# Optimization experiments

Hardware: AMD Instinct MI355X
Metric: run time of the kernel (lower is better)

## Reference

```python
import math
import jax, jax.numpy as jnp
import numpy as np

N_HEAD = 16
ROPE_BASE = 10000.0


def _qk_norm(x, scale):
    # RMSNorm over head_dim, eps added inside sqrt as in the torch code
    norm = jnp.sqrt(jnp.mean(x.astype(jnp.float32) ** 2, axis=-1, keepdims=True) + 1e-6)
    return (x.astype(jnp.float32) / norm * scale).astype(x.dtype)


def _rope3d(q, k, coords, token_type):
    # q,k: [B,H,T,D]; coords: [B,T,3]; token_type: [B,T]
    # head_dim is split into 3 equal chunks, chunk i rotated by coords[...,i].
    # Tokens with token_type == 0 (e.g. text tokens) are left unrotated.
    B, H, T, D = q.shape
    d3 = D // 3
    half = d3 // 2
    inv_freq = ROPE_BASE ** (-jnp.arange(half, dtype=jnp.float32) / half)  # [half]

    def rotate(x):
        # x: [B,H,T,D] -> rotate each of the 3 axis-chunks
        chunks = []
        for a in range(3):
            xa = x[..., a * d3:(a + 1) * d3]                       # [B,H,T,d3]
            ang = coords[:, None, :, a, None] * inv_freq            # [B,1,T,half]
            cos, sin = jnp.cos(ang), jnp.sin(ang)
            x1, x2 = xa[..., :half], xa[..., half:]
            chunks.append(jnp.concatenate([x1 * cos - x2 * sin,
                                           x1 * sin + x2 * cos], axis=-1))
        rot = jnp.concatenate(chunks, axis=-1)
        apply = (token_type > 0)[:, None, :, None]                  # [B,1,T,1]
        return jnp.where(apply, rot, x)

    return rotate(q), rotate(k)


def setup_inputs() -> dict:
    key = jax.random.key(0)
    ks = jax.random.split(key, 5)
    B, T, C = 2, 2048, 1536
    D = C // N_HEAD
    return {
        "x": jax.random.normal(ks[0], (B, T, C), jnp.float32),
        "coords": jax.random.uniform(ks[1], (B, T, 3), jnp.float32) * 32.0,
        "token_type": jax.random.randint(ks[2], (B, T), 0, 2),
        "W_qkv": jax.random.normal(ks[3], (3 * C, C), jnp.float32) * (1.0 / math.sqrt(C)),
        "W_out": jax.random.normal(ks[4], (C, C), jnp.float32) * (1.0 / math.sqrt(C)),
        "q_scale": jnp.ones((D,), jnp.float32),
        "k_scale": jnp.ones((D,), jnp.float32),
    }


def reference(x, coords, token_type, W_qkv, W_out, q_scale, k_scale):
    B, T, C = x.shape
    H = N_HEAD
    D = C // H
    qkv = x @ W_qkv.T                                   # [B,T,3C]
    q, k, v = jnp.split(qkv, 3, axis=-1)
    q = q.reshape(B, T, H, D).transpose(0, 2, 1, 3)     # [B,H,T,D]
    k = k.reshape(B, T, H, D).transpose(0, 2, 1, 3)
    v = v.reshape(B, T, H, D).transpose(0, 2, 1, 3)
    q = _qk_norm(q, q_scale)
    k = _qk_norm(k, k_scale)
    q, k = _rope3d(q, k, coords, token_type)
    scale = 1.0 / math.sqrt(D)
    attn = jnp.einsum('bhqd,bhkd->bhqk', q, k) * scale  # [B,H,T,T]
    causal = jnp.tril(jnp.ones((T, T), bool))
    attn = jnp.where(causal, attn, -jnp.inf)
    attn = jax.nn.softmax(attn, axis=-1)
    out = jnp.einsum('bhqk,bhkd->bhqd', attn, v)        # [B,H,T,D]
    out = out.transpose(0, 2, 1, 3).reshape(B, T, C)
    return out @ W_out.T
```

## Files before the change

### kernel.cpp

```cpp
#include <hip/hip_runtime.h>
#include <stdint.h>
#include <stddef.h>


typedef __attribute__((ext_vector_type(8))) __bf16 bf16x8;
typedef __attribute__((ext_vector_type(4))) __bf16 bf16x4;
typedef __attribute__((ext_vector_type(4))) float  f32x4;

#define NB 2
#define NT 2048
#define NC 1536
#define NH 16
#define ND 96
#define NQKV 4608
#define NM 4096
#define NR_BLOCKS 16384

static __device__ __forceinline__ float fexp2(float x) {
#if __has_builtin(__builtin_amdgcn_exp2f)
  return __builtin_amdgcn_exp2f(x);
#else
  return exp2f(x);
#endif
}

static __device__ __forceinline__ void g2lds16(const void* g, void* l) {
  __builtin_amdgcn_global_load_lds(
      (const __attribute__((address_space(1))) void*)g,
      (__attribute__((address_space(3))) void*)l, 16, 0, 0);
}

__global__ __launch_bounds__(256) void cvt3_f32_bf16(
    const float4* __restrict__ sx, bf16x4* __restrict__ dx, int n4x,
    const float4* __restrict__ sw, bf16x4* __restrict__ dw, int n4w,
    const float4* __restrict__ so, bf16x4* __restrict__ do_) {
  int i = blockIdx.x * 256 + threadIdx.x;
  const float4* s;
  bf16x4* d;
  if (i < n4x)            { s = sx + i;               d = dx + i; }
  else if (i < n4x + n4w) { s = sw + (i - n4x);       d = dw + (i - n4x); }
  else                    { s = so + (i - n4x - n4w); d = do_ + (i - n4x - n4w); }
  float4 v = *s;
  bf16x4 o;
  o[0] = (__bf16)v.x; o[1] = (__bf16)v.y;
  o[2] = (__bf16)v.z; o[3] = (__bf16)v.w;
  *d = o;
}

#define BAR1() do { __builtin_amdgcn_s_barrier(); \
                    asm volatile("" ::: "memory"); } while (0)
#define BAR2() do { asm volatile("" ::: "memory"); \
                    __builtin_amdgcn_s_barrier(); } while (0)
#define WAITLGKM() do { asm volatile("s_waitcnt lgkmcnt(0)" ::: "memory"); \
                        __builtin_amdgcn_sched_barrier(0); } while (0)
#define WAITVM6() asm volatile("s_waitcnt vmcnt(6)" ::: "memory")
#define WAITVM5() asm volatile("s_waitcnt vmcnt(5)" ::: "memory")

template <int MH>
static __device__ __forceinline__ void readA2(
    bf16x8 (&aR)[2][2], const char* buf, int aro, int sk0, int sk1) {
#pragma unroll
  for (int i = 0; i < 2; ++i) {
    const char* p = buf + aro + (MH * 2 + i) * 2048;
    aR[i][0] = *(const bf16x8*)(p + sk0);
    aR[i][1] = *(const bf16x8*)(p + sk1);
  }
}
template <int NF0, int NN>
static __device__ __forceinline__ void readBN(
    bf16x8 (&bb)[NN][2], const char* buf, int bro, int sk0, int sk1) {
#pragma unroll
  for (int j = 0; j < NN; ++j) {
    const char* p = buf + bro + (NF0 + j) * 2048;
    bb[j][0] = *(const bf16x8*)(p + sk0);
    bb[j][1] = *(const bf16x8*)(p + sk1);
  }
}
template <int MH, int NF0, int NN>
static __device__ __forceinline__ void quadN(
    f32x4 (&acc)[4][9], const bf16x8 (&aR)[2][2], const bf16x8 (&bb)[NN][2]) {
  __builtin_amdgcn_s_setprio(1);
#pragma unroll
  for (int i = 0; i < 2; ++i)
#pragma unroll
    for (int j = 0; j < NN; ++j)
#pragma unroll
      for (int ks = 0; ks < 2; ++ks)
        acc[MH * 2 + i][NF0 + j] = __builtin_amdgcn_mfma_f32_16x16x32_bf16(
            aR[i][ks], bb[j][ks], acc[MH * 2 + i][NF0 + j], 0, 0, 0);
  __builtin_amdgcn_s_setprio(0);
}

__global__ __launch_bounds__(512, 2) void gemm1_8ph(
    const __bf16* __restrict__ A, const __bf16* __restrict__ Bw,
    __bf16* __restrict__ C, int M, int N, int K) {
  __shared__ __align__(16) char lds[139264];
  char* const A0 = lds;
  char* const A1 = lds + 32768;
  char* const B0 = lds + 65536;
  char* const B1 = lds + 102400;

  const int tid = threadIdx.x;
  const int l   = tid & 63;
  const int w   = tid >> 6;
  const int wm  = w >> 1;
  const int wn  = w & 1;
  const int lm  = l & 15;
  const int lq  = l >> 4;

  const int nnt = 16;
  const int nwg = gridDim.x * gridDim.y;
  const int lid = blockIdx.y * gridDim.x + blockIdx.x;
  const int swz = (lid & 7) * (nwg >> 3) + (lid >> 3);
  const int m0  = (swz / nnt) * 256;
  const int n0  = (swz % nnt) * 288;

  const int aro = (wm * 64 + lm) * 128;
  const int bro = (wn * 144 + lm) * 128;
  const int sk0 = ((lq) ^ (lm & 7)) * 16;
  const int sk1 = ((4 + lq) ^ (lm & 7)) * 16;

  const int ssl = ((l & 7) ^ ((l >> 3) & 7)) * 8;
  auto stageA = [&](int grow0, int k0, char* dst) {
#pragma unroll
    for (int q2 = 0; q2 < 2; ++q2) {
      const int c   = w * 2 + q2;
      const int row = c * 8 + (l >> 3);
      g2lds16(A + (size_t)(grow0 + row) * K + k0 + ssl, dst + c * 1024);
    }
  };
  auto stageB = [&](int grow0, int k0, char* dst) {
#pragma unroll
    for (int q2 = 0; q2 < 2; ++q2) {
      const int c   = w * 2 + q2;
      const int row = c * 8 + (l >> 3);
      g2lds16(Bw + (size_t)(grow0 + row) * K + k0 + ssl, dst + c * 1024);
    }
    if (w < 2) {
      const int c   = 16 + w;
      const int row = c * 8 + (l >> 3);
      g2lds16(Bw + (size_t)(grow0 + row) * K + k0 + ssl, dst + c * 1024);
    }
  };

  f32x4 acc[4][9] = {};
  bf16x8 aL[2][2], aH[2][2], b5[5][2], b4[4][2];

  stageA(m0,       0,  A0);
  stageA(m0 + 128, 0,  A0 + 16384);
  stageB(n0,       0,  B0);
  stageB(n0 + 144, 0,  B0 + 18432);
  stageA(m0,       64, A1);
  stageA(m0 + 128, 64, A1 + 16384);

  const int NIT = K >> 7;
  for (int it = 0; it < NIT; ++it) {
    const int kh  = it * 128 + 64;
    const int knl = it * 128 + 128;
    const int knh = it * 128 + 192;
    stageB(n0, kh, B1);
    WAITVM6();
    BAR1();
    readA2<0>(aL, A0, aro, sk0, sk1);
    readBN<0, 5>(b5, B0, bro, sk0, sk1);
    WAITLGKM();
    quadN<0, 0, 5>(acc, aL, b5);
    BAR2();
    stageB(n0 + 144, kh, B1 + 18432);
    BAR1();
    readA2<1>(aH, A0, aro, sk0, sk1);
    WAITLGKM();
    quadN<1, 0, 5>(acc, aH, b5);
    BAR2();
    stageA(m0, knl, A0);
    BAR1();
    readBN<5, 4>(b4, B0, bro, sk0, sk1);
    WAITLGKM();
    quadN<1, 5, 4>(acc, aH, b4);
    BAR2();
    stageA(m0 + 128, knl, A0 + 16384);
    BAR1();
    quadN<0, 5, 4>(acc, aL, b4);
    BAR2();
    stageB(n0, knl, B0);
    WAITVM6();
    BAR1();
    readA2<0>(aL, A1, aro, sk0, sk1);
    readBN<0, 5>(b5, B1, bro, sk0, sk1);
    WAITLGKM();
    quadN<0, 0, 5>(acc, aL, b5);
    BAR2();
    stageB(n0 + 144, knl, B0 + 18432);
    BAR1();
    readA2<1>(aH, A1, aro, sk0, sk1);
    WAITLGKM();
    quadN<1, 0, 5>(acc, aH, b5);
    BAR2();
    stageA(m0, knh, A1);
    BAR1();
    readBN<5, 4>(b4, B1, bro, sk0, sk1);
    WAITLGKM();
    quadN<1, 5, 4>(acc, aH, b4);
    BAR2();
    stageA(m0 + 128, knh, A1 + 16384);
    BAR1();
    quadN<0, 5, 4>(acc, aL, b4);
    BAR2();
  }

  const int r0 = lq * 4;
#pragma unroll
  for (int mf = 0; mf < 4; ++mf)
#pragma unroll
    for (int nf = 0; nf < 9; ++nf)
#pragma unroll
      for (int r = 0; r < 4; ++r) {
        const size_t row = (size_t)(m0 + wm * 64 + mf * 16 + r0 + r);
        const size_t col = (size_t)(n0 + wn * 144 + nf * 16 + lm);
        C[row * N + col] = (__bf16)acc[mf][nf][r];
      }
}

template <int MH, int NF0, int NN>
static __device__ __forceinline__ void g2quad(
    f32x4 (&acc)[4][3], const bf16x8 (&aR)[2][2], const bf16x8 (&bb)[NN][2]) {
  __builtin_amdgcn_s_setprio(1);
#pragma unroll
  for (int i = 0; i < 2; ++i)
#pragma unroll
    for (int j = 0; j < NN; ++j)
#pragma unroll
      for (int ks = 0; ks < 2; ++ks)
        acc[MH * 2 + i][NF0 + j] = __builtin_amdgcn_mfma_f32_16x16x32_bf16(
            aR[i][ks], bb[j][ks], acc[MH * 2 + i][NF0 + j], 0, 0, 0);
  __builtin_amdgcn_s_setprio(0);
}

__global__ __launch_bounds__(512, 2) void gemm2_8ph(
    const __bf16* __restrict__ A, const __bf16* __restrict__ Bw,
    float* __restrict__ C, int M, int N, int K) {
  __shared__ __align__(16) char lds[81920];
  char* const A0 = lds;
  char* const A1 = lds + 16384;
  char* const B0 = lds + 32768;
  char* const B1 = lds + 57344;

  const int tid = threadIdx.x;
  const int l   = tid & 63;
  const int w   = tid >> 6;
  const int wm  = w >> 2;
  const int wn  = w & 3;
  const int lm  = l & 15;
  const int lq  = l >> 4;

  const int nwg = gridDim.x * gridDim.y;
  const int lid = blockIdx.y * gridDim.x + blockIdx.x;
  const int swz = (lid & 7) * (nwg >> 3) + (lid >> 3);
  const int m0  = (swz / 8) * 128;
  const int n0  = (swz % 8) * 192;

  const int aro = (wm * 64 + lm) * 128;
  const int bro = (wn * 48 + lm) * 128;
  const int sk0 = ((lq) ^ (lm & 7)) * 16;
  const int sk1 = ((4 + lq) ^ (lm & 7)) * 16;

  const int ssl = ((l & 7) ^ ((l >> 3) & 7)) * 8;
  auto stageA = [&](int k0, char* dst) {
#pragma unroll
    for (int q2 = 0; q2 < 2; ++q2) {
      const int c   = w * 2 + q2;
      const int row = c * 8 + (l >> 3);
      g2lds16(A + (size_t)(m0 + row) * K + k0 + ssl, dst + c * 1024);
    }
  };
  auto stageB = [&](int k0, char* dst) {
#pragma unroll
    for (int q2 = 0; q2 < 3; ++q2) {
      const int c   = w * 3 + q2;
      const int row = c * 8 + (l >> 3);
      g2lds16(Bw + (size_t)(n0 + row) * K + k0 + ssl, dst + c * 1024);
    }
  };

  f32x4 acc[4][3] = {};
  bf16x8 aL[2][2], aH[2][2], bL[2][2], bH[1][2];

  stageA(0,  A0);
  stageB(0,  B0);
  stageA(64, A1);

  const int NIT = K >> 7;
  for (int it = 0; it < NIT; ++it) {
    const int kh  = it * 128 + 64;
    const int knl = it * 128 + 128;
    const int knh = it * 128 + 192;
    stageB(kh, B1);
    WAITVM5();
    BAR1();
    readA2<0>(aL, A0, aro, sk0, sk1);
    readBN<0, 2>(bL, B0, bro, sk0, sk1);
    WAITLGKM();
    g2quad<0, 0, 2>(acc, aL, bL);
    BAR2();
    BAR1();
    readA2<1>(aH, A0, aro, sk0, sk1);
    WAITLGKM();
    g2quad<1, 0, 2>(acc, aH, bL);
    BAR2();
    stageA(knl, A0);
    BAR1();
    readBN<2, 1>(bH, B0, bro, sk0, sk1);
    WAITLGKM();
    g2quad<1, 2, 1>(acc, aH, bH);
    BAR2();
    BAR1();
    g2quad<0, 2, 1>(acc, aL, bH);
    BAR2();
    stageB(knl, B0);
    WAITVM5();
    BAR1();
    readA2<0>(aL, A1, aro, sk0, sk1);
    readBN<0, 2>(bL, B1, bro, sk0, sk1);
    WAITLGKM();
    g2quad<0, 0, 2>(acc, aL, bL);
    BAR2();
    BAR1();
    readA2<1>(aH, A1, aro, sk0, sk1);
    WAITLGKM();
    g2quad<1, 0, 2>(acc, aH, bL);
    BAR2();
    stageA(knh, A1);
    BAR1();
    readBN<2, 1>(bH, B1, bro, sk0, sk1);
    WAITLGKM();
    g2quad<1, 2, 1>(acc, aH, bH);
    BAR2();
    BAR1();
    g2quad<0, 2, 1>(acc, aL, bH);
    BAR2();
  }

  const int r0 = lq * 4;
#pragma unroll
  for (int mf = 0; mf < 4; ++mf)
#pragma unroll
    for (int nf = 0; nf < 3; ++nf)
#pragma unroll
      for (int r = 0; r < 4; ++r) {
        const size_t row = (size_t)(m0 + wm * 64 + mf * 16 + r0 + r);
        const size_t col = (size_t)(n0 + wn * 48 + nf * 16 + lm);
        C[row * N + col] = acc[mf][nf][r];
      }
}

static __device__ __forceinline__ float rope_one(float v, float p, int d,
                                                 const float* c3) {
  const int a  = d >> 5;
  const int j  = d & 31;
  const int jj = j & 15;
  const float invf = fexp2((float)jj * -0.8304820237218406f);
  const float ang  = c3[a] * invf;
  float sn, cs;
  __sincosf(ang, &sn, &cs);
  return (j < 16) ? (v * cs - p * sn) : (v * cs + p * sn);
}

__global__ __launch_bounds__(256) void normrope_tv(
    const __bf16* __restrict__ qkv, const float* __restrict__ coords,
    const int* __restrict__ ttype, const float* __restrict__ qsc,
    const float* __restrict__ ksc, __bf16* __restrict__ qo,
    __bf16* __restrict__ ko, __bf16* __restrict__ vo) {
  __shared__ __align__(16) __bf16 tile[96][72];
  if ((int)blockIdx.x < NR_BLOCKS) {
    const int l   = threadIdx.x & 63;
    const int w   = threadIdx.x >> 6;
    const int rid = blockIdx.x * 4 + w;
    const int h   = rid & (NH - 1);
    const int bt  = rid >> 4;
    const int t   = bt & (NT - 1);
    const int b   = bt >> 11;
    const __bf16* base = qkv + (size_t)bt * NQKV + h * ND;
    const float*  c3   = coords + (size_t)bt * 3;
    const bool rope    = ttype[bt] > 0;
    const size_t bh    = (size_t)(b * NH + h);

    {
      float x0 = (float)base[l];
      float x1 = (l < 32) ? (float)base[64 + l] : 0.f;
      float ss = x0 * x0 + x1 * x1;
#pragma unroll
      for (int off = 1; off < 64; off <<= 1) ss += __shfl_xor(ss, off, 64);
      const float rn = rsqrtf(ss * (1.f / 96.f) + 1e-6f);
      x0 *= rn * qsc[l];
      if (l < 32) x1 *= rn * qsc[64 + l];
      const float p0 = __shfl_xor(x0, 16, 64);
      const float p1 = __shfl_xor(x1, 16, 64);
      if (rope) {
        x0 = rope_one(x0, p0, l, c3);
        if (l < 32) x1 = rope_one(x1, p1, 64 + l, c3);
      }
      __bf16* dst = qo + (bh * NT + t) * ND;
      dst[l] = (__bf16)x0;
      if (l < 32) dst[64 + l] = (__bf16)x1;
    }
    {
      float x0 = (float)base[NC + l];
      float x1 = (l < 32) ? (float)base[NC + 64 + l] : 0.f;
      float ss = x0 * x0 + x1 * x1;
#pragma unroll
      for (int off = 1; off < 64; off <<= 1) ss += __shfl_xor(ss, off, 64);
      const float rn = rsqrtf(ss * (1.f / 96.f) + 1e-6f);
      x0 *= rn * ksc[l];
      if (l < 32) x1 *= rn * ksc[64 + l];
      const float p0 = __shfl_xor(x0, 16, 64);
      const float p1 = __shfl_xor(x1, 16, 64);
      if (rope) {
        x0 = rope_one(x0, p0, l, c3);
        if (l < 32) x1 = rope_one(x1, p1, 64 + l, c3);
      }
      __bf16* dst = ko + (bh * NT + t) * ND;
      dst[l] = (__bf16)x0;
      if (l < 32) dst[64 + l] = (__bf16)x1;
    }
    return;
  }
  const int bx2 = blockIdx.x - NR_BLOCKS;
  const int bh  = bx2 >> 5;
  const int t0  = (bx2 & 31) * 64;
  const int tid = threadIdx.x;
  const int tok = tid & 63;
  const int grp = tid >> 6;
  const int b   = bh >> 4, h = bh & 15;
  const __bf16* src =
      qkv + ((size_t)(b * NT + t0 + tok)) * NQKV + 2 * NC + h * ND;
#pragma unroll
  for (int q2 = 0; q2 < 3; ++q2) {
    const int ch = grp * 3 + q2;
    bf16x8 v = *(const bf16x8*)(src + ch * 8);
#pragma unroll
    for (int j = 0; j < 8; ++j) tile[ch * 8 + j][tok] = v[j];
  }
  __syncthreads();
#pragma unroll
  for (int k2 = 0; k2 < 3; ++k2) {
    const int c  = tid + k2 * 256;
    const int d  = c >> 3;
    const int tc = c & 7;
    bf16x8 v = *(const bf16x8*)(&tile[d][tc * 8]);
    *(bf16x8*)(vo + ((size_t)bh * ND + d) * NT + t0 + tc * 8) = v;
  }
}

static __device__ __forceinline__ void attn_tile64(
    const bf16x8 (&aq)[3], const bf16x8 (&bk)[4][3], int q0r, int n0,
    int lm, int lq, f32x4& lsum, __bf16* pbase ) {
  f32x4 s[4];
#pragma unroll
  for (int nt = 0; nt < 4; ++nt) {
    f32x4 a = {};
#pragma unroll
    for (int c = 0; c < 3; ++c)
      a = __builtin_amdgcn_mfma_f32_16x16x32_bf16(aq[c], bk[nt][c], a, 0, 0, 0);
    s[nt] = a;
  }
  if (n0 + 63 > q0r) {
#pragma unroll
    for (int nt = 0; nt < 4; ++nt)
#pragma unroll
      for (int r = 0; r < 4; ++r)
        if (n0 + nt * 16 + lm > q0r + lq * 4 + r) s[nt][r] = -1e30f;
  }
  const float cl = 0.10206207261596575f * 1.4426950408889634f;
#pragma unroll
  for (int nt = 0; nt < 4; ++nt)
#pragma unroll
    for (int r = 0; r < 4; ++r)
      s[nt][r] = fexp2((s[nt][r] - 96.0f) * cl);
#pragma unroll
  for (int r = 0; r < 4; ++r)
    lsum[r] += (s[0][r] + s[1][r]) + (s[2][r] + s[3][r]);
#pragma unroll
  for (int nt = 0; nt < 4; ++nt)
#pragma unroll
    for (int r = 0; r < 4; ++r)
      pbase[(nt >> 1) * 640 + (lq * 4 + r) * 40 + (nt & 1) * 16 + lm] =
          (__bf16)s[nt][r];
}

__global__ __launch_bounds__(512) void attn_fwd2(
    const __bf16* __restrict__ q, const __bf16* __restrict__ k,
    const __bf16* __restrict__ vt, __bf16* __restrict__ out) {
  __shared__ __align__(16) char KV[2][24576];
  __shared__ __align__(16) __bf16 plds[8][2][2][16][40];
  const int tid = threadIdx.x;
  const int l   = tid & 63;
  const int w   = tid >> 6;

  const int i_  = blockIdx.y * 8 + blockIdx.x;
  const int slot = i_ >> 3;
  const int bh  = (i_ & 7) + 8 * (slot & 3);
  const int qp  = slot >> 2;

  const int lm  = l & 15;
  const int lq  = l >> 4;
  const int q0L = qp * 128 + w * 16;
  const int q0H = (15 - qp) * 128 + w * 16;
  const int nktLw = qp * 2 + (w >> 2) + 1;
  const int nktHw = (15 - qp) * 2 + (w >> 2) + 1;
  const int nkt   = (15 - qp) * 2 + 2;
  const __bf16* qh = q  + (size_t)bh * NT * ND;
  const __bf16* kh = k  + (size_t)bh * NT * ND;
  const __bf16* vh = vt + (size_t)bh * ND * NT;
  __bf16* pbL = &plds[w][0][0][0][0];
  __bf16* pbH = &plds[w][1][0][0][0];

  auto stage = [&](int n0, char* buf) {
#pragma unroll
    for (int q2 = 0; q2 < 3; ++q2) {
      const int g = w * 3 + q2;
      if (g < 12) {
        const int nt = g / 3, c = g - nt * 3;
        g2lds16(kh + (size_t)(n0 + nt * 16 + (l >> 2)) * ND + c * 32 + (l & 3) * 8,
                buf + g * 1024);
      } else {
        const int gv = g - 12;
        const int dt = gv >> 1, hf = gv & 1;
        g2lds16(vh + (size_t)(dt * 16 + (l >> 2)) * NT + n0 + hf * 32 + (l & 3) * 8,
                buf + 12288 + gv * 1024);
      }
    }
  };

  bf16x8 aqL[3], aqH[3];
#pragma unroll
  for (int c = 0; c < 3; ++c) {
    aqL[c] = *(const bf16x8*)(qh + (size_t)(q0L + lm) * ND + c * 32 + lq * 8);
    aqH[c] = *(const bf16x8*)(qh + (size_t)(q0H + lm) * ND + c * 32 + lq * 8);
  }

  f32x4 oL[6] = {}, oH[6] = {};
  f32x4 lsL = {}, lsH = {};
  const int ji = (lm * 4 + lq) * 16;

  stage(0, KV[0]);
  for (int kt = 0; kt < nkt; ++kt) {
    __syncthreads();
    if (kt + 1 < nkt) stage((kt + 1) * 64, KV[(kt + 1) & 1]);
    const char* Kc = KV[kt & 1];
    const char* Vc = KV[kt & 1] + 12288;
    const int n0 = kt * 64;
    bf16x8 bk[4][3];
#pragma unroll
    for (int nt = 0; nt < 4; ++nt)
#pragma unroll
      for (int c = 0; c < 3; ++c)
        bk[nt][c] = *(const bf16x8*)(Kc + (nt * 3 + c) * 1024 + ji);
    const bool doL = kt < nktLw;
    const bool doH = kt < nktHw;
    if (doL) attn_tile64(aqL, bk, q0L, n0, lm, lq, lsL, pbL);
    if (doH) attn_tile64(aqH, bk, q0H, n0, lm, lq, lsH, pbH);
    bf16x8 apL0 = {}, apL1 = {}, apH0 = {}, apH1 = {};
    if (doL) {
      apL0 = *(const bf16x8*)(pbL + lm * 40 + lq * 8);
      apL1 = *(const bf16x8*)(pbL + 640 + lm * 40 + lq * 8);
    }
    if (doH) {
      apH0 = *(const bf16x8*)(pbH + lm * 40 + lq * 8);
      apH1 = *(const bf16x8*)(pbH + 640 + lm * 40 + lq * 8);
    }
#pragma unroll
    for (int dt = 0; dt < 6; ++dt) {
      bf16x8 bv0 = *(const bf16x8*)(Vc + (dt * 2 + 0) * 1024 + ji);
      bf16x8 bv1 = *(const bf16x8*)(Vc + (dt * 2 + 1) * 1024 + ji);
      if (doL) {
        oL[dt] = __builtin_amdgcn_mfma_f32_16x16x32_bf16(apL0, bv0, oL[dt], 0, 0, 0);
        oL[dt] = __builtin_amdgcn_mfma_f32_16x16x32_bf16(apL1, bv1, oL[dt], 0, 0, 0);
      }
      if (doH) {
        oH[dt] = __builtin_amdgcn_mfma_f32_16x16x32_bf16(apH0, bv0, oH[dt], 0, 0, 0);
        oH[dt] = __builtin_amdgcn_mfma_f32_16x16x32_bf16(apH1, bv1, oH[dt], 0, 0, 0);
      }
    }
  }

  const int b = bh >> 4, h = bh & 15;
#pragma unroll
  for (int f = 0; f < 2; ++f) {
    const f32x4* o = f ? oH : oL;
    const f32x4& ls = f ? lsH : lsL;
    const int q0 = f ? q0H : q0L;
    float rl[4];
#pragma unroll
    for (int r = 0; r < 4; ++r) {
      float v = ls[r];
#pragma unroll
      for (int off = 1; off < 16; off <<= 1) v += __shfl_xor(v, off, 64);
      rl[r] = 1.f / v;
    }
#pragma unroll
    for (int dt = 0; dt < 6; ++dt)
#pragma unroll
      for (int r = 0; r < 4; ++r) {
        const int t = q0 + lq * 4 + r;
        out[((size_t)(b * NT + t)) * NC + h * ND + dt * 16 + lm] =
            (__bf16)(o[dt][r] * rl[r]);
      }
  }
}

static constexpr size_t OFF_XB   = 0;
static constexpr size_t OFF_WQKV = 12582912;
static constexpr size_t OFF_WOUT = 26738688;
static constexpr size_t OFF_QKV  = 31457280;
static constexpr size_t OFF_Q    = 69206016;
static constexpr size_t OFF_K    = 81788928;
static constexpr size_t OFF_VT   = 94371840;

extern "C" void kernel_launch(void* const* d_in, const int* in_sizes, int n_in,
                              void* d_out, int out_size, void* d_ws,
                              size_t ws_size, hipStream_t stream) {
  const float* x      = (const float*)d_in[0];
  const float* coords = (const float*)d_in[1];
  const int*   ttype  = (const int*)d_in[2];
  const float* wqkv   = (const float*)d_in[3];
  const float* wout   = (const float*)d_in[4];
  const float* qs     = (const float*)d_in[5];
  const float* ks     = (const float*)d_in[6];

  char* ws = (char*)d_ws;
  __bf16* xb    = (__bf16*)(ws + OFF_XB);
  __bf16* wqkvb = (__bf16*)(ws + OFF_WQKV);
  __bf16* woutb = (__bf16*)(ws + OFF_WOUT);
  __bf16* qkvb  = (__bf16*)(ws + OFF_QKV);
  __bf16* qb    = (__bf16*)(ws + OFF_Q);
  __bf16* kb    = (__bf16*)(ws + OFF_K);
  __bf16* vtb   = (__bf16*)(ws + OFF_VT);
  __bf16* attnb = (__bf16*)(ws + OFF_XB);

  {
    const int n4x = NM * NC / 4;
    const int n4w = NQKV * NC / 4;
    const int n4o = NC * NC / 4;
    const int nblk = (n4x + n4w + n4o) / 256;
    cvt3_f32_bf16<<<nblk, 256, 0, stream>>>(
        (const float4*)x, (bf16x4*)xb, n4x,
        (const float4*)wqkv, (bf16x4*)wqkvb, n4w,
        (const float4*)wout, (bf16x4*)woutb);
  }
  gemm1_8ph<<<dim3(NQKV / 288, NM / 256), 512, 0, stream>>>(
      xb, wqkvb, qkvb, NM, NQKV, NC);
  normrope_tv<<<NR_BLOCKS + 1024, 256, 0, stream>>>(
      qkvb, coords, ttype, qs, ks, qb, kb, vtb);
  attn_fwd2<<<dim3(8, NB * NH), 512, 0, stream>>>(qb, kb, vtb, attnb);
  gemm2_8ph<<<dim3(NC / 192, NM / 128), 512, 0, stream>>>(
      attnb, woutb, (float*)d_out, NM, NC, NC);
}
```

Before: 284.1 us.

## Split paired causal attention tiles into one q-tile per block with higher occupancy

Replaces the paired low/high query-tile scheme with one 128-row query tile per block, doubling the grid and ordering blocks longest-first for causal load balance. Register pressure is reduced by dropping the second accumulator set and loading K fragments per MFMA, and launch bounds request 4 blocks per CU. The trade-off is that K/V tiles staged into LDS are no longer shared between two query tiles, increasing global/LDS traffic per unit of work.

```diff
diff --git a/kernel.cpp b/kernel.cpp
--- a/kernel.cpp
+++ b/kernel.cpp
@@ -451,68 +451,28 @@
   }
 }
 
-static __device__ __forceinline__ void attn_tile64(
-    const bf16x8 (&aq)[3], const bf16x8 (&bk)[4][3], int q0r, int n0,
-    int lm, int lq, f32x4& lsum, __bf16* pbase ) {
-  f32x4 s[4];
-#pragma unroll
-  for (int nt = 0; nt < 4; ++nt) {
-    f32x4 a = {};
-#pragma unroll
-    for (int c = 0; c < 3; ++c)
-      a = __builtin_amdgcn_mfma_f32_16x16x32_bf16(aq[c], bk[nt][c], a, 0, 0, 0);
-    s[nt] = a;
-  }
-  if (n0 + 63 > q0r) {
-#pragma unroll
-    for (int nt = 0; nt < 4; ++nt)
-#pragma unroll
-      for (int r = 0; r < 4; ++r)
-        if (n0 + nt * 16 + lm > q0r + lq * 4 + r) s[nt][r] = -1e30f;
-  }
-  const float cl = 0.10206207261596575f * 1.4426950408889634f;
-#pragma unroll
-  for (int nt = 0; nt < 4; ++nt)
-#pragma unroll
-    for (int r = 0; r < 4; ++r)
-      s[nt][r] = fexp2((s[nt][r] - 96.0f) * cl);
-#pragma unroll
-  for (int r = 0; r < 4; ++r)
-    lsum[r] += (s[0][r] + s[1][r]) + (s[2][r] + s[3][r]);
-#pragma unroll
-  for (int nt = 0; nt < 4; ++nt)
-#pragma unroll
-    for (int r = 0; r < 4; ++r)
-      pbase[(nt >> 1) * 640 + (lq * 4 + r) * 40 + (nt & 1) * 16 + lm] =
-          (__bf16)s[nt][r];
-}
-
-__global__ __launch_bounds__(512) void attn_fwd2(
+__global__ __launch_bounds__(512, 4) void attn_fwd3(
     const __bf16* __restrict__ q, const __bf16* __restrict__ k,
     const __bf16* __restrict__ vt, __bf16* __restrict__ out) {
   __shared__ __align__(16) char KV[2][24576];
-  __shared__ __align__(16) __bf16 plds[8][2][2][16][40];
+  __shared__ __align__(16) __bf16 plds[8][2][16][40];
   const int tid = threadIdx.x;
   const int l   = tid & 63;
   const int w   = tid >> 6;
-
-  const int i_  = blockIdx.y * 8 + blockIdx.x;
-  const int slot = i_ >> 3;
-  const int bh  = (i_ & 7) + 8 * (slot & 3);
-  const int qp  = slot >> 2;
+  const int bx  = blockIdx.x;
+  const int by  = blockIdx.y;
+  const int bh  = bx + 8 * (by & 3);
+  const int qp  = 15 - (by >> 2);
 
   const int lm  = l & 15;
   const int lq  = l >> 4;
-  const int q0L = qp * 128 + w * 16;
-  const int q0H = (15 - qp) * 128 + w * 16;
-  const int nktLw = qp * 2 + (w >> 2) + 1;
-  const int nktHw = (15 - qp) * 2 + (w >> 2) + 1;
-  const int nkt   = (15 - qp) * 2 + 2;
+  const int q0  = qp * 128 + w * 16;
+  const int nktw = qp * 2 + (w >> 2) + 1;
+  const int nkt  = qp * 2 + 2;
   const __bf16* qh = q  + (size_t)bh * NT * ND;
   const __bf16* kh = k  + (size_t)bh * NT * ND;
   const __bf16* vh = vt + (size_t)bh * ND * NT;
-  __bf16* pbL = &plds[w][0][0][0][0];
-  __bf16* pbH = &plds[w][1][0][0][0];
+  __bf16* pb = &plds[w][0][0][0];
 
   auto stage = [&](int n0, char* buf) {
 #pragma unroll
@@ -531,16 +491,15 @@
     }
   };
 
-  bf16x8 aqL[3], aqH[3];
-#pragma unroll
-  for (int c = 0; c < 3; ++c) {
-    aqL[c] = *(const bf16x8*)(qh + (size_t)(q0L + lm) * ND + c * 32 + lq * 8);
-    aqH[c] = *(const bf16x8*)(qh + (size_t)(q0H + lm) * ND + c * 32 + lq * 8);
-  }
-
-  f32x4 oL[6] = {}, oH[6] = {};
-  f32x4 lsL = {}, lsH = {};
+  bf16x8 aq[3];
+#pragma unroll
+  for (int c = 0; c < 3; ++c)
+    aq[c] = *(const bf16x8*)(qh + (size_t)(q0 + lm) * ND + c * 32 + lq * 8);
+
+  f32x4 o[6] = {};
+  f32x4 ls = {};
   const int ji = (lm * 4 + lq) * 16;
+  const float cl = 0.10206207261596575f * 1.4426950408889634f;
 
   stage(0, KV[0]);
   for (int kt = 0; kt < nkt; ++kt) {
@@ -549,63 +508,69 @@
     const char* Kc = KV[kt & 1];
     const char* Vc = KV[kt & 1] + 12288;
     const int n0 = kt * 64;
-    bf16x8 bk[4][3];
-#pragma unroll
-    for (int nt = 0; nt < 4; ++nt)
-#pragma unroll
-      for (int c = 0; c < 3; ++c)
-        bk[nt][c] = *(const bf16x8*)(Kc + (nt * 3 + c) * 1024 + ji);
-    const bool doL = kt < nktLw;
-    const bool doH = kt < nktHw;
-    if (doL) attn_tile64(aqL, bk, q0L, n0, lm, lq, lsL, pbL);
-    if (doH) attn_tile64(aqH, bk, q0H, n0, lm, lq, lsH, pbH);
-    bf16x8 apL0 = {}, apL1 = {}, apH0 = {}, apH1 = {};
-    if (doL) {
-      apL0 = *(const bf16x8*)(pbL + lm * 40 + lq * 8);
-      apL1 = *(const bf16x8*)(pbL + 640 + lm * 40 + lq * 8);
-    }
-    if (doH) {
-      apH0 = *(const bf16x8*)(pbH + lm * 40 + lq * 8);
-      apH1 = *(const bf16x8*)(pbH + 640 + lm * 40 + lq * 8);
-    }
-#pragma unroll
-    for (int dt = 0; dt < 6; ++dt) {
-      bf16x8 bv0 = *(const bf16x8*)(Vc + (dt * 2 + 0) * 1024 + ji);
-      bf16x8 bv1 = *(const bf16x8*)(Vc + (dt * 2 + 1) * 1024 + ji);
-      if (doL) {
-        oL[dt] = __builtin_amdgcn_mfma_f32_16x16x32_bf16(apL0, bv0, oL[dt], 0, 0, 0);
-        oL[dt] = __builtin_amdgcn_mfma_f32_16x16x32_bf16(apL1, bv1, oL[dt], 0, 0, 0);
-      }
-      if (doH) {
-        oH[dt] = __builtin_amdgcn_mfma_f32_16x16x32_bf16(apH0, bv0, oH[dt], 0, 0, 0);
-        oH[dt] = __builtin_amdgcn_mfma_f32_16x16x32_bf16(apH1, bv1, oH[dt], 0, 0, 0);
+    const bool doW = kt < nktw;
+    if (doW) {
+      f32x4 s[4];
+#pragma unroll
+      for (int nt = 0; nt < 4; ++nt) {
+        f32x4 a = {};
+#pragma unroll
+        for (int c = 0; c < 3; ++c) {
+          bf16x8 bk = *(const bf16x8*)(Kc + (nt * 3 + c) * 1024 + ji);
+          a = __builtin_amdgcn_mfma_f32_16x16x32_bf16(aq[c], bk, a, 0, 0, 0);
+        }
+        s[nt] = a;
+      }
+      if (n0 + 63 > q0) {
+#pragma unroll
+        for (int nt = 0; nt < 4; ++nt)
+#pragma unroll
+          for (int r = 0; r < 4; ++r)
+            if (n0 + nt * 16 + lm > q0 + lq * 4 + r) s[nt][r] = -1e30f;
+      }
+#pragma unroll
+      for (int nt = 0; nt < 4; ++nt)
+#pragma unroll
+        for (int r = 0; r < 4; ++r)
+          s[nt][r] = fexp2((s[nt][r] - 96.0f) * cl);
+#pragma unroll
+      for (int r = 0; r < 4; ++r)
+        ls[r] += (s[0][r] + s[1][r]) + (s[2][r] + s[3][r]);
+#pragma unroll
+      for (int nt = 0; nt < 4; ++nt)
+#pragma unroll
+        for (int r = 0; r < 4; ++r)
+          pb[(nt >> 1) * 640 + (lq * 4 + r) * 40 + (nt & 1) * 16 + lm] =
+              (__bf16)s[nt][r];
+      bf16x8 ap0 = *(const bf16x8*)(pb + lm * 40 + lq * 8);
+      bf16x8 ap1 = *(const bf16x8*)(pb + 640 + lm * 40 + lq * 8);
+#pragma unroll
+      for (int dt = 0; dt < 6; ++dt) {
+        bf16x8 bv0 = *(const bf16x8*)(Vc + (dt * 2 + 0) * 1024 + ji);
+        bf16x8 bv1 = *(const bf16x8*)(Vc + (dt * 2 + 1) * 1024 + ji);
+        o[dt] = __builtin_amdgcn_mfma_f32_16x16x32_bf16(ap0, bv0, o[dt], 0, 0, 0);
+        o[dt] = __builtin_amdgcn_mfma_f32_16x16x32_bf16(ap1, bv1, o[dt], 0, 0, 0);
       }
     }
   }
 
   const int b = bh >> 4, h = bh & 15;
-#pragma unroll
-  for (int f = 0; f < 2; ++f) {
-    const f32x4* o = f ? oH : oL;
-    const f32x4& ls = f ? lsH : lsL;
-    const int q0 = f ? q0H : q0L;
-    float rl[4];
+  float rl[4];
+#pragma unroll
+  for (int r = 0; r < 4; ++r) {
+    float v = ls[r];
+#pragma unroll
+    for (int off = 1; off < 16; off <<= 1) v += __shfl_xor(v, off, 64);
+    rl[r] = 1.f / v;
+  }
+#pragma unroll
+  for (int dt = 0; dt < 6; ++dt)
 #pragma unroll
     for (int r = 0; r < 4; ++r) {
-      float v = ls[r];
-#pragma unroll
-      for (int off = 1; off < 16; off <<= 1) v += __shfl_xor(v, off, 64);
-      rl[r] = 1.f / v;
-    }
-#pragma unroll
-    for (int dt = 0; dt < 6; ++dt)
-#pragma unroll
-      for (int r = 0; r < 4; ++r) {
-        const int t = q0 + lq * 4 + r;
-        out[((size_t)(b * NT + t)) * NC + h * ND + dt * 16 + lm] =
-            (__bf16)(o[dt][r] * rl[r]);
-      }
-  }
+      const int t = q0 + lq * 4 + r;
+      out[((size_t)(b * NT + t)) * NC + h * ND + dt * 16 + lm] =
+          (__bf16)(o[dt][r] * rl[r]);
+    }
 }
 
 static constexpr size_t OFF_XB   = 0;
@@ -651,7 +616,7 @@
       xb, wqkvb, qkvb, NM, NQKV, NC);
   normrope_tv<<<NR_BLOCKS + 1024, 256, 0, stream>>>(
       qkvb, coords, ttype, qs, ks, qb, kb, vtb);
-  attn_fwd2<<<dim3(8, NB * NH), 512, 0, stream>>>(qb, kb, vtb, attnb);
+  attn_fwd3<<<dim3(8, 64), 512, 0, stream>>>(qb, kb, vtb, attnb);
   gemm2_8ph<<<dim3(NC / 192, NM / 128), 512, 0, stream>>>(
       attnb, woutb, (float*)d_out, NM, NC, NC);
 }
```

Result: no change. 289.1 us (+1.8%).
